# Optimization experiments

Measured on AMD Instinct MI355X. Metric: run time of the kernel, lower is better.

Reference implementation:

```python
import jax, jax.numpy as jnp
import numpy as np
from jax import lax

WINDOW_SIZES = (3, 5, 7)
FEATURE_SCALES = (1.0, 1.0, 0.5, 0.001)  # mean, variance, skewness, kurtosis
EPS = 1e-8


def _gaussian_window(k: int) -> jnp.ndarray:
    sigma = k / 6.0
    coords = jnp.arange(k, dtype=jnp.float32) - (k // 2)
    g = jnp.exp(-coords ** 2 / (2.0 * sigma ** 2))
    g = g / g.sum()
    g2 = g[None, :] * g[:, None]
    return g2 / g2.sum()  # [k, k]


def _dwconv(x: jnp.ndarray, w2d: jnp.ndarray) -> jnp.ndarray:
    # depthwise conv, same gaussian kernel for every channel, SAME-style padding k//2
    c = x.shape[1]
    k = w2d.shape[-1]
    kernel = jnp.broadcast_to(w2d[None, None], (c, 1, k, k)).astype(x.dtype)
    p = k // 2
    return lax.conv_general_dilated(
        x, kernel, window_strides=(1, 1), padding=[(p, p), (p, p)],
        dimension_numbers=('NCHW', 'OIHW', 'NCHW'), feature_group_count=c)


def _stat_features(x: jnp.ndarray, w2d: jnp.ndarray):
    mean = _dwconv(x, w2d)
    var = jnp.clip(_dwconv(x * x, w2d) - mean * mean, EPS, None)
    xc = x - mean
    m3 = _dwconv(xc * xc * xc, w2d)
    m4 = _dwconv(xc * xc * xc * xc, w2d)
    std = jnp.sqrt(var)
    skew = m3 / (std * std * std + EPS)
    kurt = m4 / (var * var + EPS)
    return (mean, var, skew, kurt)


def setup_inputs() -> dict:
    key = jax.random.key(0)
    k1, k2 = jax.random.split(key)
    pred = jax.random.normal(k1, (16, 3, 512, 512), dtype=jnp.float32)
    target = jax.random.normal(k2, (16, 3, 512, 512), dtype=jnp.float32)
    return {"pred": pred, "target": target}


def reference(pred, target):
    loss_weight = 1.0
    total = jnp.asarray(0.0, dtype=pred.dtype)
    num_features = 0
    for k in WINDOW_SIZES:
        w2d = _gaussian_window(k)
        pf = _stat_features(pred, w2d)
        tf = _stat_features(target, w2d)
        for p_feat, t_feat, scale in zip(pf, tf, FEATURE_SCALES):
            total = total + jnp.abs(p_feat - t_feat).mean() * scale
            num_features += 1
    return loss_weight * total / num_features
```

## Files before the change

### kernel.cpp

```cpp
#include <hip/hip_runtime.h>
#include <math.h>


static constexpr int H = 512, W = 512, PLANES = 48;
static constexpr float EPSF = 1e-8f;

__global__ void init_acc_kernel(double* acc) {
    if (threadIdx.x < 4) acc[threadIdx.x] = 0.0;
}

__global__ void final_kernel(const double* __restrict__ acc, float* __restrict__ out) {
    if (threadIdx.x == 0) {
        const double npix = (double)PLANES * H * W;
        double tot = acc[0] + acc[1] + 0.5 * acc[2] + 0.001 * acc[3];
        out[0] = (float)(tot / (npix * 12.0));
    }
}

__device__ __forceinline__ float bperm(int addr, float v) {
    return __int_as_float(__builtin_amdgcn_ds_bpermute(addr, __float_as_int(v)));
}

#define STAT_ITER(I_, U_)                                                      \
  {                                                                            \
    const int ii = (I_);                                                       \
    const int uu = (U_);                                                       \
    const int yrow = y0 + ii;                                                  \
    const float rmask = (((unsigned)(yrow - R) < (unsigned)H) ? 1.f : 0.f) * colmask; \
    _Pragma("unroll")                                                          \
    for (int s = 0; s < 2; ++s) {                                              \
      const float x = pfbuf[s][uu % P];                                        \
      pfbuf[s][uu % P] = loadrow(s, yrow + P);                                 \
      xr[s][uu % DX] = x;                                                      \
      float w[K];                                                              \
      _Pragma("unroll")                                                        \
      for (int j = 0; j < K; ++j) w[j] = (j == R) ? x : bperm(adrb + 4 * j, x); \
      float hx = 0.f, hq = 0.f;                                                \
      _Pragma("unroll")                                                        \
      for (int j = 0; j < K; ++j) { hx += g[j] * w[j]; hq += g[j] * (w[j] * w[j]); } \
      _Pragma("unroll")                                                        \
      for (int d = 0; d < K; ++d) {                                            \
        const int sl = (uu + d - R + 2 * D) % D;                               \
        if (d == K - 1) { mn[s][sl] = g[d] * hx; msq[s][sl] = g[d] * hq; }     \
        else           { mn[s][sl] += g[d] * hx; msq[s][sl] += g[d] * hq; }    \
      }                                                                        \
      const float xold  = xr[s][(uu - R + 2 * DX) % DX];                       \
      const float mean1 = mn[s][(uu - R + 2 * D) % D];                         \
      const float xcm   = (xold - mean1) * rmask;                              \
      float wc[K];                                                             \
      _Pragma("unroll")                                                        \
      for (int j = 0; j < K; ++j) wc[j] = (j == R) ? xcm : bperm(adrb + 4 * j, xcm); \
      float v3 = 0.f, v4 = 0.f;                                                \
      _Pragma("unroll")                                                        \
      for (int j = 0; j < K; ++j) {                                            \
        const float c2 = wc[j] * wc[j];                                        \
        v3 += g[j] * (c2 * wc[j]);                                             \
        v4 += g[j] * (c2 * c2);                                                \
      }                                                                        \
      _Pragma("unroll")                                                        \
      for (int d = 0; d < K; ++d) {                                            \
        const int sl = (uu + d - 2 * R + 2 * D) % D;                           \
        if (d == K - 1) { m3a[s][sl] = g[d] * v3; m4a[s][sl] = g[d] * v4; }    \
        else           { m3a[s][sl] += g[d] * v3; m4a[s][sl] += g[d] * v4; }   \
      }                                                                        \
      if (ii >= 4 * R && ii < T) {                                             \
        const int se = (uu - 2 * R + 2 * D) % D;                               \
        const float mean = mn[s][se];                                          \
        const float var  = fmaxf(msq[s][se] - mean * mean, EPSF);              \
        const float sd   = sqrtf(var);                                         \
        const float skew = __fdividef(m3a[s][se], sd * var + EPSF);            \
        const float kurt = __fdividef(m4a[s][se], var * var + EPSF);           \
        if (s == 0) {                                                          \
          featp[0] = mean; featp[1] = var; featp[2] = skew; featp[3] = kurt;   \
        } else {                                                               \
          sums[0] += fabsf(featp[0] - mean);                                   \
          sums[1] += fabsf(featp[1] - var);                                    \
          sums[2] += fabsf(featp[2] - skew);                                   \
          sums[3] += fabsf(featp[3] - kurt);                                   \
        }                                                                      \
      }                                                                        \
    }                                                                          \
  }

template <int K, int BAND, int D, int DX, int P, int NSTRIP>
__global__ __launch_bounds__(256)
void stat_kernel(const float* __restrict__ pred, const float* __restrict__ targ,
                 double* __restrict__ acc) {
    constexpr int R  = K / 2;
    constexpr int OW = 64 - 4 * R;
    constexpr int NBAND = H / BAND;
    constexpr int T  = BAND + 4 * R;
    constexpr int Tp = ((T + D - 1) / D) * D;
    static_assert(D % P == 0 && D % DX == 0, "index folding needs P|D, DX|D");
    static_assert(D >= 3 * R + 1 && DX > R, "ring lifetimes");

    const int wv    = threadIdx.x >> 6;
    const int wid   = blockIdx.x * 4 + wv;
    const int band  = wid % NBAND;
    const int tmp   = wid / NBAND;
    const int strip = tmp % NSTRIP;
    const int plane = tmp / NSTRIP;
    const int t     = threadIdx.x & 63;
    const int gc0   = strip * OW - 2 * R + t;
    const int y0    = band * BAND - 2 * R;

    const bool  iva     = (unsigned)gc0 < (unsigned)W;
    const float colmask = iva ? 1.f : 0.f;
    const float emask   = (t >= 2 * R && t < 2 * R + OW && gc0 < W) ? 1.f : 0.f;

    const int adrb = (t - R) << 2;

    float g[K];
    {
        const float sigma = (float)K / 6.0f;
        const float inv2s2 = 1.0f / (2.0f * sigma * sigma);
        float s = 0.0f;
#pragma unroll
        for (int i = 0; i < K; ++i) {
            float c = (float)(i - K / 2);
            g[i] = expf(-c * c * inv2s2);
            s += g[i];
        }
#pragma unroll
        for (int i = 0; i < K; ++i)
            g[i] = __int_as_float(__builtin_amdgcn_readfirstlane(__float_as_int(g[i] / s)));
    }

    const unsigned ibase = (unsigned)(plane * (H * W) + gc0);

    auto loadrow = [&](int s, int y) -> float {
        float v = 0.f;
        if (iva && (unsigned)y < (unsigned)H)
            v = (s == 0 ? pred : targ)[ibase + ((unsigned)y << 9)];
        return v;
    };

    float mn[2][D], msq[2][D], m3a[2][D], m4a[2][D], xr[2][DX];
    float pfbuf[2][P];
    float featp[4];
    float sums[4] = {0.f, 0.f, 0.f, 0.f};

#pragma unroll
    for (int j = 0; j < P; ++j) {
        pfbuf[0][j] = loadrow(0, y0 + j);
        pfbuf[1][j] = loadrow(1, y0 + j);
    }

    for (int yy = 0; yy < Tp; yy += D) {
#pragma unroll
        for (int u = 0; u < D; ++u) {
            STAT_ITER(yy + u, u)
        }
    }

    __shared__ float red[4][4];
#pragma unroll
    for (int f = 0; f < 4; ++f) {
        float v = sums[f] * emask;
#pragma unroll
        for (int off = 32; off > 0; off >>= 1) v += __shfl_down(v, off, 64);
        if (t == 0) red[wv][f] = v;
    }
    __syncthreads();
    if (threadIdx.x < 4) {
        float v = red[0][threadIdx.x] + red[1][threadIdx.x]
                + red[2][threadIdx.x] + red[3][threadIdx.x];
        atomicAdd(&acc[threadIdx.x], (double)v);
    }
}

extern "C" void kernel_launch(void* const* d_in, const int* in_sizes, int n_in,
                              void* d_out, int out_size, void* d_ws, size_t ws_size,
                              hipStream_t stream) {
    const float* pred = (const float*)d_in[0];
    const float* targ = (const float*)d_in[1];
    double* acc = (double*)d_ws;
    float* out = (float*)d_out;

    init_acc_kernel<<<1, 64, 0, stream>>>(acc);

    stat_kernel<3, 32,  4, 2, 4,  9><<<dim3(PLANES *  9 * 16 / 4), 256, 0, stream>>>(pred, targ, acc);
    stat_kernel<5, 32,  8, 4, 4, 10><<<dim3(PLANES * 10 * 16 / 4), 256, 0, stream>>>(pred, targ, acc);
    stat_kernel<7, 32, 10, 5, 5, 10><<<dim3(PLANES * 10 * 16 / 4), 256, 0, stream>>>(pred, targ, acc);

    final_kernel<<<1, 64, 0, stream>>>(acc, out);
}
```

Before: 463.2 us.

## Software-pipeline the centered-moment stage for K=7 and retune K=5 ring sizes

Adds a pipelined variant of the per-row statistics step that computes the centered-value horizontal shuffles one iteration ahead, so the third- and fourth-moment passes overlap with the mean and variance pass. Skew and kurtosis now divide by denominators cached from the previous row. The variant is enabled only for the 7x7 window, which needs one extra iteration of lag. Separately, the ring depth, row-window and prefetch sizes for the 5x5 kernel change from 8/4/4 to 7/7/7. The extra live arrays raise register pressure and could lower occupancy.

```diff
diff --git a/kernel.cpp b/kernel.cpp
--- a/kernel.cpp
+++ b/kernel.cpp
@@ -82,7 +82,74 @@
     }                                                                          \
   }
 
-template <int K, int BAND, int D, int DX, int P, int NSTRIP>
+#define STAT_ITER_PP(I_, U_)                                                   \
+  {                                                                            \
+    const int ii = (I_);                                                       \
+    const int uu = (U_);                                                       \
+    const int yrow = y0 + ii;                                                  \
+    const float rmask = (((unsigned)(yrow - R) < (unsigned)H) ? 1.f : 0.f) * colmask; \
+    float w[2][K];                                                             \
+    _Pragma("unroll")                                                          \
+    for (int s = 0; s < 2; ++s) {                                              \
+      const float xa = pfbuf[s][uu % P];                                       \
+      pfbuf[s][uu % P] = loadrow(s, yrow + P);                                 \
+      xr[s][uu % DX] = xa;                                                     \
+      _Pragma("unroll")                                                        \
+      for (int j = 0; j < K; ++j) w[s][j] = (j == R) ? xa : bperm(adrb + 4 * j, xa); \
+    }                                                                          \
+    _Pragma("unroll")                                                          \
+    for (int s = 0; s < 2; ++s) {                                              \
+      float v3 = 0.f, v4 = 0.f;                                                \
+      _Pragma("unroll")                                                        \
+      for (int j = 0; j < K; ++j) {                                            \
+        const float c2 = wcp[s][j] * wcp[s][j];                                \
+        v3 += g[j] * (c2 * wcp[s][j]);                                         \
+        v4 += g[j] * (c2 * c2);                                                \
+      }                                                                        \
+      _Pragma("unroll")                                                        \
+      for (int d = 0; d < K; ++d) {                                            \
+        const int sl = (uu - 1 + d - 2 * R + 3 * D) % D;                       \
+        if (d == K - 1) { m3a[s][sl] = g[d] * v3; m4a[s][sl] = g[d] * v4; }    \
+        else           { m3a[s][sl] += g[d] * v3; m4a[s][sl] += g[d] * v4; }   \
+      }                                                                        \
+      if (ii >= 4 * R + 1 && ii <= T) {                                        \
+        const int sesk = (uu - 1 - 2 * R + 3 * D) % D;                         \
+        const float skew = __fdividef(m3a[s][sesk], denS[s]);                  \
+        const float kurt = __fdividef(m4a[s][sesk], denK[s]);                  \
+        if (s == 0) { fsk0 = skew; fsk1 = kurt; }                              \
+        else { sums[2] += fabsf(fsk0 - skew); sums[3] += fabsf(fsk1 - kurt); } \
+      }                                                                        \
+    }                                                                          \
+    _Pragma("unroll")                                                          \
+    for (int s = 0; s < 2; ++s) {                                              \
+      float hx = 0.f, hq = 0.f;                                                \
+      _Pragma("unroll")                                                        \
+      for (int j = 0; j < K; ++j) { hx += g[j] * w[s][j]; hq += g[j] * (w[s][j] * w[s][j]); } \
+      _Pragma("unroll")                                                        \
+      for (int d = 0; d < K; ++d) {                                            \
+        const int sl = (uu + d - R + 2 * D) % D;                               \
+        if (d == K - 1) { mn[s][sl] = g[d] * hx; msq[s][sl] = g[d] * hq; }     \
+        else           { mn[s][sl] += g[d] * hx; msq[s][sl] += g[d] * hq; }    \
+      }                                                                        \
+      if (ii >= 4 * R && ii < T) {                                             \
+        const int se = (uu - 2 * R + 2 * D) % D;                               \
+        const float mean = mn[s][se];                                          \
+        const float var  = fmaxf(msq[s][se] - mean * mean, EPSF);              \
+        const float sd   = sqrtf(var);                                         \
+        denS[s] = sd * var + EPSF;                                             \
+        denK[s] = var * var + EPSF;                                            \
+        if (s == 0) { fmv0 = mean; fmv1 = var; }                               \
+        else { sums[0] += fabsf(fmv0 - mean); sums[1] += fabsf(fmv1 - var); }  \
+      }                                                                        \
+      const float xold  = xr[s][(uu - R + 2 * DX) % DX];                       \
+      const float mean1 = mn[s][(uu - R + 2 * D) % D];                         \
+      const float xcm   = (xold - mean1) * rmask;                              \
+      _Pragma("unroll")                                                        \
+      for (int j = 0; j < K; ++j) wcp[s][j] = (j == R) ? xcm : bperm(adrb + 4 * j, xcm); \
+    }                                                                          \
+  }
+
+template <int K, int BAND, int D, int DX, int P, int NSTRIP, int PIPE>
 __global__ __launch_bounds__(256)
 void stat_kernel(const float* __restrict__ pred, const float* __restrict__ targ,
                  double* __restrict__ acc) {
@@ -90,7 +157,7 @@
     constexpr int OW = 64 - 4 * R;
     constexpr int NBAND = H / BAND;
     constexpr int T  = BAND + 4 * R;
-    constexpr int Tp = ((T + D - 1) / D) * D;
+    constexpr int Tp = ((T + D - 1 + PIPE) / D) * D;
     static_assert(D % P == 0 && D % DX == 0, "index folding needs P|D, DX|D");
     static_assert(D >= 3 * R + 1 && DX > R, "ring lifetimes");
 
@@ -138,6 +205,9 @@
     float mn[2][D], msq[2][D], m3a[2][D], m4a[2][D], xr[2][DX];
     float pfbuf[2][P];
     float featp[4];
+    float wcp[2][K] = {};
+    float denS[2] = {1.f, 1.f}, denK[2] = {1.f, 1.f};
+    float fsk0 = 0.f, fsk1 = 0.f, fmv0 = 0.f, fmv1 = 0.f;
     float sums[4] = {0.f, 0.f, 0.f, 0.f};
 
 #pragma unroll
@@ -149,7 +219,8 @@
     for (int yy = 0; yy < Tp; yy += D) {
 #pragma unroll
         for (int u = 0; u < D; ++u) {
-            STAT_ITER(yy + u, u)
+            if constexpr (PIPE) { STAT_ITER_PP(yy + u, u) }
+            else                { STAT_ITER(yy + u, u) }
         }
     }
 
@@ -179,9 +250,9 @@
 
     init_acc_kernel<<<1, 64, 0, stream>>>(acc);
 
-    stat_kernel<3, 32,  4, 2, 4,  9><<<dim3(PLANES *  9 * 16 / 4), 256, 0, stream>>>(pred, targ, acc);
-    stat_kernel<5, 32,  8, 4, 4, 10><<<dim3(PLANES * 10 * 16 / 4), 256, 0, stream>>>(pred, targ, acc);
-    stat_kernel<7, 32, 10, 5, 5, 10><<<dim3(PLANES * 10 * 16 / 4), 256, 0, stream>>>(pred, targ, acc);
+    stat_kernel<3, 32,  4, 2, 4,  9, 0><<<dim3(PLANES *  9 * 16 / 4), 256, 0, stream>>>(pred, targ, acc);
+    stat_kernel<5, 32,  7, 7, 7, 10, 0><<<dim3(PLANES * 10 * 16 / 4), 256, 0, stream>>>(pred, targ, acc);
+    stat_kernel<7, 32, 10, 5, 5, 10, 1><<<dim3(PLANES * 10 * 16 / 4), 256, 0, stream>>>(pred, targ, acc);
 
     final_kernel<<<1, 64, 0, stream>>>(acc, out);
 }
```

Result: slower. 493.2 us (+6.5%).
